# Kernel optimization log

Hardware: AMD Instinct MI355X
Metric: run time of the kernel (lower is better)

Reference implementation:

```python
import jax, jax.numpy as jnp
import numpy as np

B, N, F_IN = 8, 1024, 128
H, F_OUT = 4, 64
NEG_INF = -9e15


def setup_inputs() -> dict:
    key = jax.random.key(0)
    k1, k2, k3, k4 = jax.random.split(key, 4)
    x = jax.random.normal(k1, (B, N, F_IN), dtype=jnp.float32)
    adj = jax.random.randint(k2, (B, N, N), 0, 2, dtype=jnp.int32)
    W = jax.random.normal(k3, (F_IN, H * F_OUT), dtype=jnp.float32) * 0.05
    a = jax.random.normal(k4, (H, 2 * F_OUT), dtype=jnp.float32)
    return {"x": x, "adj": adj, "W": W, "a": a}


def reference(x, adj, W, a):
    # x: [B,N,F_in], adj: [B,N,N], W: [F_in, H*F_out], a: [H, 2*F_out]
    Bs, Ns, _ = x.shape
    Hh = a.shape[0]
    Fo = a.shape[1] // 2
    h = (x @ W).reshape(Bs, Ns, Hh, Fo)            # [B,N,H,F]
    # e_{bnmh} = a . cat(h_i, h_j) = a_src . h_n + a_dst . h_m  (no O(N^2) concat)
    a_src, a_dst = a[:, :Fo], a[:, Fo:]
    e_src = jnp.einsum('bnhf,hf->bnh', h, a_src)    # [B,N,H]
    e_dst = jnp.einsum('bmhf,hf->bmh', h, a_dst)    # [B,N,H]
    e = e_src[:, :, None, :] + e_dst[:, None, :, :]  # [B,N,N,H]
    e = jax.nn.leaky_relu(e, negative_slope=0.2)
    e = jnp.where(adj[..., None] > 0, e, NEG_INF)
    attention = jax.nn.softmax(e, axis=2)           # softmax over neighbors m
    h_prime = jnp.einsum('bnmh,bmhf->bnhf', attention, h)
    return h_prime.mean(axis=2)                     # [B,N,F_out]
```

## Files before the change

### kernel.cpp

```cpp
#include <hip/hip_runtime.h>
#include <math.h>

#define Bsz 8
#define Nsz 1024
#define FIN 128
#define Hh  4
#define FO  64
#define COLS 256
#define TN  16
#define TM  32
#define BN  (Bsz*Nsz)
#define SHIFT 12.0f
#define HSTR 40
#define PSTR 136
#define XSTR 136

typedef __attribute__((ext_vector_type(8))) short short8;
typedef __attribute__((ext_vector_type(4))) float f32x4;

static __device__ inline ushort f2bf(float f) {
    uint u = __float_as_uint(f);
    u += 0x7FFFu + ((u >> 16) & 1u);
    return (ushort)(u >> 16);
}
static __device__ inline float bf2f(ushort h) { return __uint_as_float(((uint)h) << 16); }

__global__ __launch_bounds__(256) void gat_prep(const float* __restrict__ W,
                                                ushort* __restrict__ Wt)
{
    const int g = blockIdx.x * 256 + threadIdx.x;
    const int n = g >> 3, kc = (g & 7) * 16;
    ushort u[16];
    #pragma unroll
    for (int i = 0; i < 16; i++) u[i] = f2bf(W[(kc + i) * COLS + n]);
    int4* dst = (int4*)(Wt + n * FIN + kc);
    dst[0] = ((int4*)u)[0];
    dst[1] = ((int4*)u)[1];
}

__global__ __launch_bounds__(256) void gat_proj(
    const float* __restrict__ x, const ushort* __restrict__ Wt,
    const float* __restrict__ a, ushort* __restrict__ h_gB,
    float* __restrict__ es_g, float* __restrict__ ed_g)
{
    __shared__ ushort xs[16 * XSTR];
    const int j    = threadIdx.x;
    const int w    = j >> 6, lane = j & 63, quad = lane >> 4, n16 = lane & 15;
    const int b    = blockIdx.x >> 6, mt16 = blockIdx.x & 63;
    const long rowbase = (long)b * Nsz + mt16 * 16;

    short8 bfr[4][4];
    #pragma unroll
    for (int kk = 0; kk < 4; kk++)
        #pragma unroll
        for (int c4 = 0; c4 < 4; c4++)
            bfr[kk][c4] = *(const short8*)(Wt + (w*64 + c4*16 + n16) * FIN + kk*32 + quad*8);

    {
        const int r = j >> 4, k0 = (j & 15) * 8;
        const float4* g4 = (const float4*)(x + (rowbase + r) * FIN + k0);
        float4 v0 = g4[0], v1 = g4[1];
        ushort u[8] = { f2bf(v0.x), f2bf(v0.y), f2bf(v0.z), f2bf(v0.w),
                        f2bf(v1.x), f2bf(v1.y), f2bf(v1.z), f2bf(v1.w) };
        *(int4*)(xs + r * XSTR + k0) = *(int4*)u;
    }
    __syncthreads();

    f32x4 acc[4];
    #pragma unroll
    for (int c4 = 0; c4 < 4; c4++)
        #pragma unroll
        for (int r = 0; r < 4; r++) acc[c4][r] = 0.f;

    #pragma unroll
    for (int kk = 0; kk < 4; kk++) {
        short8 af = *(const short8*)(xs + n16 * XSTR + kk*32 + quad*8);
        #pragma unroll
        for (int c4 = 0; c4 < 4; c4++)
            acc[c4] = __builtin_amdgcn_mfma_f32_16x16x32_bf16(af, bfr[kk][c4], acc[c4], 0, 0, 0);
    }

    const int mtile = mt16 >> 1;
    const int kbase = (mt16 & 1) * 16 + quad * 4;
    #pragma unroll
    for (int c4 = 0; c4 < 4; c4++) {
        uint2 pk;
        pk.x = (uint)f2bf(acc[c4][0]) | ((uint)f2bf(acc[c4][1]) << 16);
        pk.y = (uint)f2bf(acc[c4][2]) | ((uint)f2bf(acc[c4][3]) << 16);
        const int c = w*64 + c4*16 + n16;
        *(uint2*)(h_gB + (((long)(b*32 + mtile) * COLS + c) * 32 + kbase)) = pk;
    }

    float aS[4], aD[4];
    #pragma unroll
    for (int c4 = 0; c4 < 4; c4++) {
        aS[c4] = a[w * (2*FO) + c4*16 + n16];
        aD[c4] = a[w * (2*FO) + FO + c4*16 + n16];
    }
    #pragma unroll
    for (int reg = 0; reg < 4; reg++) {
        float ps = 0.f, pd = 0.f;
        #pragma unroll
        for (int c4 = 0; c4 < 4; c4++) {
            ps = fmaf(acc[c4][reg], aS[c4], ps);
            pd = fmaf(acc[c4][reg], aD[c4], pd);
        }
        #pragma unroll
        for (int off = 1; off < 16; off <<= 1) {
            ps += __shfl_xor(ps, off, 64);
            pd += __shfl_xor(pd, off, 64);
        }
        if (n16 == 0) {
            const long row = rowbase + quad*4 + reg;
            es_g[(long)w * BN + row] = ps;
            ed_g[(long)w * BN + row] = pd;
        }
    }
}

__global__ __launch_bounds__(256, 3) void gat_attn(
    const int* __restrict__ adj, const ushort* __restrict__ h_gB,
    const float* __restrict__ es_g, const float* __restrict__ ed_g,
    float* __restrict__ out)
{
    __shared__ ushort hT[2][COLS * HSTR];
    __shared__ ushort pT[2][TN * PSTR];
    __shared__ float  l_lds[TN * Hh];

    const int j    = threadIdx.x;
    const int w    = j >> 6, lane = j & 63, quad = lane >> 4, n16 = lane & 15;
    const int mi   = lane & 31, hh = lane >> 5;
    const int b    = blockIdx.y;
    const int n0   = blockIdx.x * TN;
    const long rowb = (long)b * Nsz + n0;

    float es[4][2];
    #pragma unroll
    for (int r4 = 0; r4 < 4; r4++)
        #pragma unroll
        for (int ii = 0; ii < 2; ii++)
            es[r4][ii] = es_g[(long)(hh*2 + ii) * BN + rowb + w*4 + r4];

    f32x4 acc[4];
    #pragma unroll
    for (int c4 = 0; c4 < 4; c4++)
        #pragma unroll
        for (int r = 0; r < 4; r++) acc[c4][r] = 0.f;

    float l_part[4][2];
    #pragma unroll
    for (int r4 = 0; r4 < 4; r4++) { l_part[r4][0] = 0.f; l_part[r4][1] = 0.f; }

    short8 hreg[4]; int areg[4]; float edreg[2];
    const short8* hb8 = (const short8*)h_gB;

#define PREFETCH(t) {                                                           \
    const short8* g = hb8 + (long)(b*32 + (t)) * 1024;                          \
    hreg[0] = g[j]; hreg[1] = g[j+256]; hreg[2] = g[j+512]; hreg[3] = g[j+768]; \
    const int m0p = (t) * TM;                                                   \
    _Pragma("unroll")                                                           \
    for (int r4 = 0; r4 < 4; r4++)                                              \
        areg[r4] = adj[(rowb + w*4 + r4) * (long)Nsz + m0p + mi];               \
    _Pragma("unroll")                                                           \
    for (int ii = 0; ii < 2; ii++)                                              \
        edreg[ii] = ed_g[(long)(hh*2 + ii) * BN + (long)b * Nsz + m0p + mi]; }

#define STAGE(buf) {                                                            \
    _Pragma("unroll")                                                           \
    for (int i = 0; i < 4; i++) {                                               \
        const int s = j + 256*i;                                                \
        *(short8*)(&hT[buf][(s >> 2) * HSTR + (s & 3) * 8]) = hreg[i]; } }

#define PHASE_S(buf) {                                                          \
    _Pragma("unroll")                                                           \
    for (int r4 = 0; r4 < 4; r4++) {                                            \
        _Pragma("unroll")                                                       \
        for (int ii = 0; ii < 2; ii++) {                                        \
            float s = es[r4][ii] + edreg[ii];                                   \
            s = fmaxf(s, 0.2f * s);                                             \
            float p = (areg[r4] > 0) ? __expf(s - SHIFT) : 0.f;                 \
            ushort pb = f2bf(p);                                                \
            pT[buf][(w*4 + r4) * PSTR + (hh*2 + ii) * TM + mi] = pb;            \
            l_part[r4][ii] += bf2f(pb); } } }

#define PHASE_A(buf) {                                                          \
    short8 af = *(const short8*)(&pT[buf][n16 * PSTR + w * TM + quad * 8]);     \
    _Pragma("unroll")                                                           \
    for (int c4 = 0; c4 < 4; c4++) {                                            \
        short8 bfv = *(const short8*)(&hT[buf][(w*64 + c4*16 + n16) * HSTR + quad * 8]); \
        acc[c4] = __builtin_amdgcn_mfma_f32_16x16x32_bf16(af, bfv, acc[c4], 0, 0, 0); } }

    PREFETCH(0);
    STAGE(0); PHASE_S(0);
    PREFETCH(1);
    __syncthreads();

    for (int t = 0; t < Nsz / TM; t++) {
        const int cur = t & 1;
        if (t < Nsz / TM - 1) {
            STAGE(cur ^ 1);
            PHASE_S(cur ^ 1);
            if (t < Nsz / TM - 2) PREFETCH(t + 2);
        }
        PHASE_A(cur);
        __syncthreads();
    }

    #pragma unroll
    for (int r4 = 0; r4 < 4; r4++)
        #pragma unroll
        for (int ii = 0; ii < 2; ii++) {
            float lp = l_part[r4][ii];
            #pragma unroll
            for (int off = 1; off < 32; off <<= 1) lp += __shfl_xor(lp, off, 64);
            if (mi == 0) l_lds[(w*4 + r4) * Hh + hh*2 + ii] = lp;
        }
    __syncthreads();

    float* o_lds = (float*)&hT[0][0];
    float rinv[4];
    #pragma unroll
    for (int reg = 0; reg < 4; reg++)
        rinv[reg] = 0.25f / l_lds[(quad*4 + reg) * Hh + w];
    #pragma unroll
    for (int c4 = 0; c4 < 4; c4++)
        #pragma unroll
        for (int reg = 0; reg < 4; reg++)
            o_lds[(w * TN + quad*4 + reg) * FO + c4*16 + n16] = acc[c4][reg] * rinv[reg];
    __syncthreads();

    {
        const int f2 = j & 63, rb = j >> 6;
        #pragma unroll
        for (int i = 0; i < 4; i++) {
            const int r = i*4 + rb;
            const float sum = o_lds[(0*TN + r)*FO + f2] + o_lds[(1*TN + r)*FO + f2]
                            + o_lds[(2*TN + r)*FO + f2] + o_lds[(3*TN + r)*FO + f2];
            out[(rowb + r) * FO + f2] = sum;
        }
    }
#undef PREFETCH
#undef STAGE
#undef PHASE_S
#undef PHASE_A
}

extern "C" void kernel_launch(void* const* d_in, const int* in_sizes, int n_in,
                              void* d_out, int out_size, void* d_ws, size_t ws_size,
                              hipStream_t stream) {
    const float* x   = (const float*)d_in[0];
    const int*   adj = (const int*)d_in[1];
    const float* W   = (const float*)d_in[2];
    const float* a   = (const float*)d_in[3];
    float* out = (float*)d_out;

    ushort* Wt   = (ushort*)d_ws;
    ushort* h_gB = Wt + (size_t)COLS * FIN;
    float*  es_g = (float*)(h_gB + (size_t)BN * COLS);
    float*  ed_g = es_g + (size_t)Hh * BN;

    gat_prep<<<dim3(8),            dim3(256), 0, stream>>>(W, Wt);
    gat_proj<<<dim3(Bsz*Nsz/16),   dim3(256), 0, stream>>>(x, Wt, a, h_gB, es_g, ed_g);
    gat_attn<<<dim3(Nsz/TN, Bsz),  dim3(256), 0, stream>>>(adj, h_gB, es_g, ed_g, out);
}
```

Baseline: 114.5 us.

## Deepen attention prefetch, vectorize score math, and drop LDS staging in projection

The attention kernel now keeps two register prefetch slots and unrolls the tile loop by two, so global loads for tile t+3 are in flight while tile t is consumed. The score phase uses packed float2 arithmetic and packed bf16 conversions, and the launch-bounds occupancy hint drops from 3 to 2 blocks per SM so more registers are available. The projection kernel loads x directly into MFMA fragments and skips the shared-memory staging and barrier. The extra prefetch registers raise register pressure and reduce occupancy, which can offset the gain in latency hiding.

```diff
diff --git a/kernel.cpp b/kernel.cpp
--- a/kernel.cpp
+++ b/kernel.cpp
@@ -1,4 +1,5 @@
 #include <hip/hip_runtime.h>
+#include <hip/hip_bf16.h>
 #include <math.h>
 
 #define Bsz 8
@@ -13,17 +14,21 @@
 #define SHIFT 12.0f
 #define HSTR 40
 #define PSTR 136
-#define XSTR 136
 
 typedef __attribute__((ext_vector_type(8))) short short8;
 typedef __attribute__((ext_vector_type(4))) float f32x4;
+typedef __attribute__((ext_vector_type(2))) float f32x2;
 
 static __device__ inline ushort f2bf(float f) {
     uint u = __float_as_uint(f);
     u += 0x7FFFu + ((u >> 16) & 1u);
     return (ushort)(u >> 16);
 }
-static __device__ inline float bf2f(ushort h) { return __uint_as_float(((uint)h) << 16); }
+static __device__ inline uint cvt_pk2(float lo, float hi) {
+    union { __hip_bfloat162 h; uint u; } cv;
+    cv.h = __float22bfloat162_rn(float2{lo, hi});
+    return cv.u;
+}
 
 __global__ __launch_bounds__(256) void gat_prep(const float* __restrict__ W,
                                                 ushort* __restrict__ Wt)
@@ -43,7 +48,6 @@
     const float* __restrict__ a, ushort* __restrict__ h_gB,
     float* __restrict__ es_g, float* __restrict__ ed_g)
 {
-    __shared__ ushort xs[16 * XSTR];
     const int j    = threadIdx.x;
     const int w    = j >> 6, lane = j & 63, quad = lane >> 4, n16 = lane & 15;
     const int b    = blockIdx.x >> 6, mt16 = blockIdx.x & 63;
@@ -56,15 +60,17 @@
         for (int c4 = 0; c4 < 4; c4++)
             bfr[kk][c4] = *(const short8*)(Wt + (w*64 + c4*16 + n16) * FIN + kk*32 + quad*8);
 
-    {
-        const int r = j >> 4, k0 = (j & 15) * 8;
-        const float4* g4 = (const float4*)(x + (rowbase + r) * FIN + k0);
-        float4 v0 = g4[0], v1 = g4[1];
-        ushort u[8] = { f2bf(v0.x), f2bf(v0.y), f2bf(v0.z), f2bf(v0.w),
-                        f2bf(v1.x), f2bf(v1.y), f2bf(v1.z), f2bf(v1.w) };
-        *(int4*)(xs + r * XSTR + k0) = *(int4*)u;
-    }
-    __syncthreads();
+    short8 af[4];
+    const float* xr = x + (rowbase + n16) * FIN + quad * 8;
+    #pragma unroll
+    for (int kk = 0; kk < 4; kk++) {
+        float4 v0 = *(const float4*)(xr + kk*32);
+        float4 v1 = *(const float4*)(xr + kk*32 + 4);
+        union { uint u[4]; short8 s; } pk;
+        pk.u[0] = cvt_pk2(v0.x, v0.y); pk.u[1] = cvt_pk2(v0.z, v0.w);
+        pk.u[2] = cvt_pk2(v1.x, v1.y); pk.u[3] = cvt_pk2(v1.z, v1.w);
+        af[kk] = pk.s;
+    }
 
     f32x4 acc[4];
     #pragma unroll
@@ -73,20 +79,18 @@
         for (int r = 0; r < 4; r++) acc[c4][r] = 0.f;
 
     #pragma unroll
-    for (int kk = 0; kk < 4; kk++) {
-        short8 af = *(const short8*)(xs + n16 * XSTR + kk*32 + quad*8);
+    for (int kk = 0; kk < 4; kk++)
         #pragma unroll
         for (int c4 = 0; c4 < 4; c4++)
-            acc[c4] = __builtin_amdgcn_mfma_f32_16x16x32_bf16(af, bfr[kk][c4], acc[c4], 0, 0, 0);
-    }
+            acc[c4] = __builtin_amdgcn_mfma_f32_16x16x32_bf16(af[kk], bfr[kk][c4], acc[c4], 0, 0, 0);
 
     const int mtile = mt16 >> 1;
     const int kbase = (mt16 & 1) * 16 + quad * 4;
     #pragma unroll
     for (int c4 = 0; c4 < 4; c4++) {
         uint2 pk;
-        pk.x = (uint)f2bf(acc[c4][0]) | ((uint)f2bf(acc[c4][1]) << 16);
-        pk.y = (uint)f2bf(acc[c4][2]) | ((uint)f2bf(acc[c4][3]) << 16);
+        pk.x = cvt_pk2(acc[c4][0], acc[c4][1]);
+        pk.y = cvt_pk2(acc[c4][2], acc[c4][3]);
         const int c = w*64 + c4*16 + n16;
         *(uint2*)(h_gB + (((long)(b*32 + mtile) * COLS + c) * 32 + kbase)) = pk;
     }
@@ -118,7 +122,7 @@
     }
 }
 
-__global__ __launch_bounds__(256, 3) void gat_attn(
+__global__ __launch_bounds__(256, 2) void gat_attn(
     const int* __restrict__ adj, const ushort* __restrict__ h_gB,
     const float* __restrict__ es_g, const float* __restrict__ ed_g,
     float* __restrict__ out)
@@ -134,12 +138,11 @@
     const int n0   = blockIdx.x * TN;
     const long rowb = (long)b * Nsz + n0;
 
-    float es[4][2];
+    f32x2 es2[4];
     #pragma unroll
     for (int r4 = 0; r4 < 4; r4++)
-        #pragma unroll
-        for (int ii = 0; ii < 2; ii++)
-            es[r4][ii] = es_g[(long)(hh*2 + ii) * BN + rowb + w*4 + r4];
+        es2[r4] = (f32x2){ es_g[(long)(hh*2 + 0) * BN + rowb + w*4 + r4],
+                           es_g[(long)(hh*2 + 1) * BN + rowb + w*4 + r4] };
 
     f32x4 acc[4];
     #pragma unroll
@@ -147,70 +150,77 @@
         #pragma unroll
         for (int r = 0; r < 4; r++) acc[c4][r] = 0.f;
 
-    float l_part[4][2];
-    #pragma unroll
-    for (int r4 = 0; r4 < 4; r4++) { l_part[r4][0] = 0.f; l_part[r4][1] = 0.f; }
-
-    short8 hreg[4]; int areg[4]; float edreg[2];
+    f32x2 l2p[4];
+    #pragma unroll
+    for (int r4 = 0; r4 < 4; r4++) l2p[r4] = (f32x2){0.f, 0.f};
+
+    short8 hr[2][4]; int ar[2][4]; f32x2 edr[2];
     const short8* hb8 = (const short8*)h_gB;
 
-#define PREFETCH(t) {                                                           \
+#define PREFETCH(t, S) {                                                        \
     const short8* g = hb8 + (long)(b*32 + (t)) * 1024;                          \
-    hreg[0] = g[j]; hreg[1] = g[j+256]; hreg[2] = g[j+512]; hreg[3] = g[j+768]; \
+    hr[S][0] = g[j];     hr[S][1] = g[j+256];                                   \
+    hr[S][2] = g[j+512]; hr[S][3] = g[j+768];                                   \
     const int m0p = (t) * TM;                                                   \
     _Pragma("unroll")                                                           \
     for (int r4 = 0; r4 < 4; r4++)                                              \
-        areg[r4] = adj[(rowb + w*4 + r4) * (long)Nsz + m0p + mi];               \
-    _Pragma("unroll")                                                           \
-    for (int ii = 0; ii < 2; ii++)                                              \
-        edreg[ii] = ed_g[(long)(hh*2 + ii) * BN + (long)b * Nsz + m0p + mi]; }
-
-#define STAGE(buf) {                                                            \
+        ar[S][r4] = adj[(rowb + w*4 + r4) * (long)Nsz + m0p + mi];              \
+    edr[S] = (f32x2){ ed_g[(long)(hh*2 + 0) * BN + (long)b * Nsz + m0p + mi],   \
+                      ed_g[(long)(hh*2 + 1) * BN + (long)b * Nsz + m0p + mi] }; }
+
+#define STAGE(buf, S) {                                                         \
     _Pragma("unroll")                                                           \
     for (int i = 0; i < 4; i++) {                                               \
         const int s = j + 256*i;                                                \
-        *(short8*)(&hT[buf][(s >> 2) * HSTR + (s & 3) * 8]) = hreg[i]; } }
-
-#define PHASE_S(buf) {                                                          \
+        *(short8*)(&hT[buf][(s >> 2) * HSTR + (s & 3) * 8]) = hr[S][i]; } }
+
+#define PHASE_S(buf, S) {                                                       \
     _Pragma("unroll")                                                           \
     for (int r4 = 0; r4 < 4; r4++) {                                            \
-        _Pragma("unroll")                                                       \
-        for (int ii = 0; ii < 2; ii++) {                                        \
-            float s = es[r4][ii] + edreg[ii];                                   \
-            s = fmaxf(s, 0.2f * s);                                             \
-            float p = (areg[r4] > 0) ? __expf(s - SHIFT) : 0.f;                 \
-            ushort pb = f2bf(p);                                                \
-            pT[buf][(w*4 + r4) * PSTR + (hh*2 + ii) * TM + mi] = pb;            \
-            l_part[r4][ii] += bf2f(pb); } } }
+        f32x2 s2 = es2[r4] + edr[S];                                            \
+        s2 = __builtin_elementwise_max(s2, s2 * 0.2f);                          \
+        s2 = s2 - SHIFT;                                                        \
+        float e0 = __expf(s2.x), e1 = __expf(s2.y);                             \
+        const bool keep = ar[S][r4] > 0;                                        \
+        uint pk = cvt_pk2(keep ? e0 : 0.f, keep ? e1 : 0.f);                    \
+        pT[buf][(w*4 + r4) * PSTR + (hh*2 + 0) * TM + mi] = (ushort)(pk & 0xFFFFu); \
+        pT[buf][(w*4 + r4) * PSTR + (hh*2 + 1) * TM + mi] = (ushort)(pk >> 16); \
+        l2p[r4] += (f32x2){ __uint_as_float(pk << 16),                          \
+                            __uint_as_float(pk & 0xFFFF0000u) }; } }
 
 #define PHASE_A(buf) {                                                          \
-    short8 af = *(const short8*)(&pT[buf][n16 * PSTR + w * TM + quad * 8]);     \
+    short8 afp = *(const short8*)(&pT[buf][n16 * PSTR + w * TM + quad * 8]);    \
     _Pragma("unroll")                                                           \
     for (int c4 = 0; c4 < 4; c4++) {                                            \
         short8 bfv = *(const short8*)(&hT[buf][(w*64 + c4*16 + n16) * HSTR + quad * 8]); \
-        acc[c4] = __builtin_amdgcn_mfma_f32_16x16x32_bf16(af, bfv, acc[c4], 0, 0, 0); } }
-
-    PREFETCH(0);
-    STAGE(0); PHASE_S(0);
-    PREFETCH(1);
+        acc[c4] = __builtin_amdgcn_mfma_f32_16x16x32_bf16(afp, bfv, acc[c4], 0, 0, 0); } }
+
+    PREFETCH(0, 0); PREFETCH(1, 1);
+    STAGE(0, 0); PHASE_S(0, 0);
+    PREFETCH(2, 0);
     __syncthreads();
 
-    for (int t = 0; t < Nsz / TM; t++) {
-        const int cur = t & 1;
-        if (t < Nsz / TM - 1) {
-            STAGE(cur ^ 1);
-            PHASE_S(cur ^ 1);
-            if (t < Nsz / TM - 2) PREFETCH(t + 2);
-        }
-        PHASE_A(cur);
+    for (int tt = 0; tt < 16; tt++) {
+        const int t0 = 2 * tt;
+        if (t0 < 31) {
+            STAGE(1, 1); PHASE_S(1, 1);
+            if (t0 + 3 < 32) PREFETCH(t0 + 3, 1);
+        }
+        PHASE_A(0);
         __syncthreads();
+        if (t0 + 1 < 31) {
+            STAGE(0, 0); PHASE_S(0, 0);
+            if (t0 + 4 < 32) PREFETCH(t0 + 4, 0);
+        }
+        PHASE_A(1);
+        __syncthreads();
     }
 
     #pragma unroll
     for (int r4 = 0; r4 < 4; r4++)
         #pragma unroll
         for (int ii = 0; ii < 2; ii++) {
-            float lp = l_part[r4][ii];
+            float lp = ii ? l2p[r4].y : l2p[r4].x;
             #pragma unroll
             for (int off = 1; off < 32; off <<= 1) lp += __shfl_xor(lp, off, 64);
             if (mi == 0) l_lds[(w*4 + r4) * Hh + hh*2 + ii] = lp;
```

Result: no change. 116.1 us (+1.4%).
